# Kernel optimization log

Hardware: AMD Instinct MI355X
Metric: run time of the kernel (lower is better)

Reference implementation:

```python
import jax, jax.numpy as jnp
import numpy as np

N = 100000   # nodes per batched graph
E = 1000000  # edges per batched graph
G = 64       # graphs in batch
D = 64       # node feature dim
H = 128      # hidden dim
L = 3        # num GCN layers
EPS = 1e-5


def setup_inputs() -> dict:
    key = jax.random.key(0)
    ks = jax.random.split(key, 20)
    def xavier(k, shape):
        fan_in, fan_out = shape[0], shape[1]
        lim = np.sqrt(6.0 / (fan_in + fan_out)).astype(np.float32)
        return jax.random.uniform(k, shape, jnp.float32, -lim, lim)
    return {
        'kernel_x': jax.random.normal(ks[0], (N, D), jnp.float32),
        'kernel_edge_index': jax.random.randint(ks[1], (2, E), 0, N, jnp.int32),
        'kernel_batch': jnp.sort(jax.random.randint(ks[2], (N,), 0, G, jnp.int32)),
        'design_x': jax.random.normal(ks[3], (N, D), jnp.float32),
        'design_edge_index': jax.random.randint(ks[4], (2, E), 0, N, jnp.int32),
        'design_batch': jnp.sort(jax.random.randint(ks[5], (N,), 0, G, jnp.int32)),
        'pragma_count': 4,
        'enc_W': xavier(ks[6], (D, H)), 'enc_b': jnp.zeros((H,), jnp.float32),
        'conv_W': jnp.stack([xavier(ks[7 + i], (H, H)) for i in range(L)]),
        'conv_b': jnp.zeros((L, H), jnp.float32),
        'ln_w': jnp.ones((L, H), jnp.float32), 'ln_b': jnp.zeros((L, H), jnp.float32),
        'head_W1': xavier(ks[10], (2 * H, H)), 'head_b1': jnp.zeros((H,), jnp.float32),
        'head_W2': xavier(ks[11], (H, H // 2)), 'head_b2': jnp.zeros((H // 2,), jnp.float32),
        'head_W3': xavier(ks[12], (H // 2, 1)), 'head_b3': jnp.zeros((1,), jnp.float32),
    }


def _gcn(x, W, b, src, dst):
    # PyG GCNConv: x' = D^{-1/2} (A + I) D^{-1/2} (x W) + b
    n = x.shape[0]
    xw = x @ W
    loop = jnp.arange(n, dtype=src.dtype)
    s = jnp.concatenate([src, loop])
    d = jnp.concatenate([dst, loop])
    deg = jax.ops.segment_sum(jnp.ones_like(d, dtype=x.dtype), d, num_segments=n)
    dinv = jax.lax.rsqrt(deg)  # deg >= 1 due to self-loops
    norm = dinv[s] * dinv[d]                       # [E+N]
    msgs = xw[s] * norm[:, None]                   # gather-transform
    return jax.ops.segment_sum(msgs, d, num_segments=n) + b


def _graph_layernorm(x, w, b, batch, num_graphs):
    # PyG LayerNorm mode='graph': normalize over all nodes+channels per graph
    n, c = x.shape
    cnt = jax.ops.segment_sum(jnp.ones((n,), x.dtype), batch, num_segments=num_graphs) * c
    mean = jax.ops.segment_sum(x.sum(axis=1), batch, num_segments=num_graphs) / cnt
    xc = x - mean[batch][:, None]
    var = jax.ops.segment_sum((xc * xc).sum(axis=1), batch, num_segments=num_graphs) / cnt
    out = xc * jax.lax.rsqrt(var + EPS)[batch][:, None]
    return out * w + b


def _encode_graph(x, edge_index, batch, enc_W, enc_b, conv_W, conv_b, ln_w, ln_b):
    src, dst = edge_index[0], edge_index[1]
    h = x @ enc_W + enc_b
    for i in range(L):
        h = _gcn(h, conv_W[i], conv_b[i], src, dst)
        h = _graph_layernorm(h, ln_w[i], ln_b[i], batch, G)
        if i < L - 1:
            h = jax.nn.relu(h)
    return jax.ops.segment_sum(h, batch, num_segments=G)  # global_add_pool -> [G, H]


def reference(kernel_x, kernel_edge_index, kernel_batch,
              design_x, design_edge_index, design_batch, pragma_count,
              enc_W, enc_b, conv_W, conv_b, ln_w, ln_b,
              head_W1, head_b1, head_W2, head_b2, head_W3, head_b3):
    design_repr = _encode_graph(design_x, design_edge_index, design_batch,
                                enc_W, enc_b, conv_W, conv_b, ln_w, ln_b)
    kernel_repr = _encode_graph(kernel_x, kernel_edge_index, kernel_batch,
                                enc_W, enc_b, conv_W, conv_b, ln_w, ln_b)
    combined = jnp.concatenate([kernel_repr, design_repr], axis=-1)  # [G, 2H]
    h = jax.nn.relu(combined @ head_W1 + head_b1)  # dropout is identity at eval
    h = jax.nn.relu(h @ head_W2 + head_b2)
    return h @ head_W3 + head_b3  # delta_pred [G, 1]
```

## Files before the change

kernel.cpp:

```cpp
#include <hip/hip_runtime.h>


#define TPB 256
#define FILL_CHUNK 2048

typedef __attribute__((ext_vector_type(8))) short bf16x8;
typedef __attribute__((ext_vector_type(4))) float f32x4;

__device__ __forceinline__ float bf2f(unsigned short s) {
  unsigned int u = ((unsigned int)s) << 16;
  float f;
  __builtin_memcpy(&f, &u, 4);
  return f;
}

__device__ __forceinline__ unsigned short f2bf(float f) {
  unsigned int u;
  __builtin_memcpy(&u, &f, 4);
  u = (u + 0x7FFF + ((u >> 16) & 1)) >> 16;
  return (unsigned short)u;
}


__global__ __launch_bounds__(TPB) void count_dst_k(const int* __restrict__ dst,
                                                   int* __restrict__ cnt, int E) {
  int e = blockIdx.x * TPB + threadIdx.x;
  if (e < E) atomicAdd(&cnt[dst[e]], 1);
}

__global__ __launch_bounds__(TPB) void prep_node_k(const int* __restrict__ cnt,
                                                   float* __restrict__ dinv,
                                                   const int* __restrict__ batch,
                                                   int* __restrict__ gstart, int n, int G) {
  int i = blockIdx.x * TPB + threadIdx.x;
  if (i >= n) return;
  dinv[i] = 1.0f / sqrtf((float)cnt[i] + 1.0f);
  int b = batch[i];
  if (i == 0) {
    for (int g = 0; g <= b; ++g) gstart[g] = 0;
  } else {
    int pb = batch[i - 1];
    for (int g = pb + 1; g <= b; ++g) gstart[g] = i;
  }
  if (i == n - 1) {
    for (int g = b + 1; g <= G; ++g) gstart[g] = n;
  }
}


__global__ __launch_bounds__(TPB) void scan_partial_k(const int* __restrict__ cnt,
                                                      int* __restrict__ bsum, int n) {
  __shared__ int sd[TPB];
  int t = threadIdx.x, i0 = blockIdx.x * 512 + t * 2;
  int s = 0;
  if (i0 < n) s += cnt[i0];
  if (i0 + 1 < n) s += cnt[i0 + 1];
  sd[t] = s;
  __syncthreads();
  for (int st = TPB / 2; st > 0; st >>= 1) {
    if (t < st) sd[t] += sd[t + st];
    __syncthreads();
  }
  if (t == 0) bsum[blockIdx.x] = sd[0];
}

__global__ __launch_bounds__(TPB) void scan_small_k(const int* __restrict__ bsum,
                                                    int* __restrict__ bpre, int P,
                                                    int* __restrict__ rowptr, int n) {
  __shared__ int sd[TPB];
  int t = threadIdx.x;
  int v = (t < P) ? bsum[t] : 0;
  sd[t] = v;
  __syncthreads();
  for (int d = 1; d < TPB; d <<= 1) {
    int w = (t >= d) ? sd[t - d] : 0;
    __syncthreads();
    sd[t] += w;
    __syncthreads();
  }
  if (t < P) bpre[t] = sd[t] - v;
  if (t == TPB - 1) rowptr[n] = sd[TPB - 1];
}

__global__ __launch_bounds__(TPB) void scan_fill_k(const int* __restrict__ cnt,
                                                   const int* __restrict__ bpre,
                                                   int* __restrict__ rowptr,
                                                   int* __restrict__ cursor, int n) {
  __shared__ int sd[TPB];
  int t = threadIdx.x, i0 = blockIdx.x * 512 + t * 2;
  int c0 = (i0 < n) ? cnt[i0] : 0;
  int c1 = (i0 + 1 < n) ? cnt[i0 + 1] : 0;
  int s = c0 + c1;
  sd[t] = s;
  __syncthreads();
  for (int d = 1; d < TPB; d <<= 1) {
    int w = (t >= d) ? sd[t - d] : 0;
    __syncthreads();
    sd[t] += w;
    __syncthreads();
  }
  int ex = sd[t] - s + bpre[blockIdx.x];
  if (i0 < n) { rowptr[i0] = ex; cursor[i0] = ex; }
  if (i0 + 1 < n) { rowptr[i0 + 1] = ex + c0; cursor[i0 + 1] = ex + c0; }
}


__global__ __launch_bounds__(TPB) void csrfill_k(const int* __restrict__ esrc,
                                                 const int* __restrict__ edst,
                                                 int* __restrict__ cursor,
                                                 int* __restrict__ csr_src, int E, int n) {
  int range = blockIdx.x & 7;
  int chunk = blockIdx.x >> 3;
  int nper = (n + 7) >> 3;
  int lo = range * nper;
  int hi = lo + nper; if (hi > n) hi = n;
  int base = chunk * FILL_CHUNK;
  int end = base + FILL_CHUNK; if (end > E) end = E;
  for (int e = base + threadIdx.x; e < end; e += TPB) {
    int d = edst[e];
    if (d >= lo && d < hi) {
      int p = atomicAdd(&cursor[d], 1);
      csr_src[p] = esrc[e];
    }
  }
}


__global__ __launch_bounds__(TPB) void wprep_k(const float* __restrict__ encW,
                                               const float* __restrict__ convW,
                                               unsigned short* __restrict__ encWt,
                                               unsigned short* __restrict__ convWt) {
  int idx = blockIdx.x * TPB + threadIdx.x;
  if (idx < 64 * 128) {
    int k = idx >> 7, c = idx & 127;
    encWt[c * 64 + k] = f2bf(encW[idx]);
  }
  idx -= 64 * 128;
  if (idx >= 0 && idx < 3 * 128 * 128) {
    int l = idx >> 14, r = idx & 16383;
    int k = r >> 7, c = r & 127;
    convWt[l * 16384 + c * 128 + k] = f2bf(convW[idx]);
  }
}


template <int K, bool BIAS, bool LNRELU, bool SCALE, bool F32IN>
__global__ __launch_bounds__(TPB) void mfma_gemm_k(
    const void* __restrict__ Av, const unsigned short* __restrict__ Wt,
    const float* __restrict__ bias, unsigned short* __restrict__ C, int nrows,
    const int* __restrict__ batch, const float* __restrict__ meanA,
    const float* __restrict__ rsigA, const float* __restrict__ lnw,
    const float* __restrict__ lnb, const float* __restrict__ dinv) {
  __shared__ short As[128 * K];
  __shared__ short Bs[128 * K];
  const int tid = threadIdx.x;
  const int r0 = blockIdx.x << 7;
  const int lane = tid & 63;
  const int wv = tid >> 6;
  const int lr = lane & 15, lg = lane >> 4;
  constexpr int CPR = K / 8;

  for (int i = tid; i < 128 * CPR; i += TPB) {
    int rloc = i / CPR, cb = i % CPR;
    int r = r0 + rloc;
    bf16x8 v = {0, 0, 0, 0, 0, 0, 0, 0};
    if (r < nrows) {
      if (F32IN) {
        const float* Af = ((const float*)Av) + (long)r * K + cb * 8;
        float4 f0 = *(const float4*)Af;
        float4 f1 = *(const float4*)(Af + 4);
        v[0] = (short)f2bf(f0.x); v[1] = (short)f2bf(f0.y);
        v[2] = (short)f2bf(f0.z); v[3] = (short)f2bf(f0.w);
        v[4] = (short)f2bf(f1.x); v[5] = (short)f2bf(f1.y);
        v[6] = (short)f2bf(f1.z); v[7] = (short)f2bf(f1.w);
      } else {
        v = *(const bf16x8*)(((const unsigned short*)Av) + (long)r * K + cb * 8);
        if (LNRELU) {
          int g = batch[r];
          float m = meanA[g], rs = rsigA[g];
          int c0 = cb * 8;
#pragma unroll
          for (int j = 0; j < 8; ++j) {
            float f = bf2f((unsigned short)v[j]);
            f = (f - m) * rs * lnw[c0 + j] + lnb[c0 + j];
            f = fmaxf(f, 0.f);
            v[j] = (short)f2bf(f);
          }
        }
      }
    }
    int sb = cb ^ (rloc & 7);
    *(bf16x8*)(&As[rloc * K + sb * 8]) = v;
  }
  for (int i = tid; i < 128 * CPR; i += TPB) {
    int rloc = i / CPR, cb = i % CPR;
    bf16x8 v = *(const bf16x8*)(Wt + (long)rloc * K + cb * 8);
    int sb = cb ^ (rloc & 7);
    *(bf16x8*)(&Bs[rloc * K + sb * 8]) = v;
  }
  __syncthreads();

  f32x4 acc[2][8];
#pragma unroll
  for (int m = 0; m < 2; ++m)
#pragma unroll
    for (int n = 0; n < 8; ++n) acc[m][n] = {0.f, 0.f, 0.f, 0.f};

  const int wrow = wv * 32;
#pragma unroll
  for (int k0 = 0; k0 < K; k0 += 32) {
    const int cbk = (k0 >> 3) + lg;
    bf16x8 a[2], b[8];
#pragma unroll
    for (int m = 0; m < 2; ++m) {
      int rr = wrow + m * 16 + lr;
      int sb = cbk ^ (rr & 7);
      a[m] = *(const bf16x8*)(&As[rr * K + sb * 8]);
    }
#pragma unroll
    for (int n = 0; n < 8; ++n) {
      int rr = n * 16 + lr;
      int sb = cbk ^ (rr & 7);
      b[n] = *(const bf16x8*)(&Bs[rr * K + sb * 8]);
    }
#pragma unroll
    for (int m = 0; m < 2; ++m)
#pragma unroll
      for (int n = 0; n < 8; ++n)
        acc[m][n] = __builtin_amdgcn_mfma_f32_16x16x32_bf16(a[m], b[n], acc[m][n], 0, 0, 0);
  }

  float bv[8];
#pragma unroll
  for (int n = 0; n < 8; ++n) bv[n] = BIAS ? bias[n * 16 + lr] : 0.f;
#pragma unroll
  for (int m = 0; m < 2; ++m) {
#pragma unroll
    for (int ri = 0; ri < 4; ++ri) {
      int r = r0 + wrow + m * 16 + lg * 4 + ri;
      if (r < nrows) {
        float dv = SCALE ? dinv[r] : 1.f;
#pragma unroll
        for (int n = 0; n < 8; ++n) {
          float v = acc[m][n][ri] + bv[n];
          if (SCALE) v *= dv;
          C[(long)r * 128 + n * 16 + lr] = f2bf(v);
        }
      }
    }
  }
}


__global__ __launch_bounds__(TPB) void aggregate_k(
    const uint4* __restrict__ xws, const int* __restrict__ rowptr,
    const int* __restrict__ csr, const float* __restrict__ dinv,
    const float* __restrict__ bias, uint4* __restrict__ outb,
    float2* __restrict__ rs2, int n) {
  int wave = threadIdx.x >> 6, lane = threadIdx.x & 63;
  int d = (blockIdx.x << 2) + wave;
  if (d >= n) return;
  const int g3 = lane >> 4, cpos = lane & 15;
  float acc[8];
#pragma unroll
  for (int j = 0; j < 8; ++j) acc[j] = 0.f;

  int p0 = rowptr[d], p1 = rowptr[d + 1];
  for (int base = p0; base < p1; base += 64) {
    int idx = base + lane;
    int sl = (idx < p1) ? csr[idx] : 0;
    int cnt = p1 - base;
    if (cnt > 64) cnt = 64;
    for (int e = 0; e < cnt; e += 8) {
      int e0 = e + g3, e1 = e + 4 + g3;
      int s0 = __shfl(sl, e0);
      int s1 = __shfl(sl, e1);
      uint4 u0 = xws[(long)s0 * 16 + cpos];
      uint4 u1 = xws[(long)s1 * 16 + cpos];
      if (e0 < cnt) {
        acc[0] += __uint_as_float(u0.x << 16);
        acc[1] += __uint_as_float(u0.x & 0xffff0000u);
        acc[2] += __uint_as_float(u0.y << 16);
        acc[3] += __uint_as_float(u0.y & 0xffff0000u);
        acc[4] += __uint_as_float(u0.z << 16);
        acc[5] += __uint_as_float(u0.z & 0xffff0000u);
        acc[6] += __uint_as_float(u0.w << 16);
        acc[7] += __uint_as_float(u0.w & 0xffff0000u);
      }
      if (e1 < cnt) {
        acc[0] += __uint_as_float(u1.x << 16);
        acc[1] += __uint_as_float(u1.x & 0xffff0000u);
        acc[2] += __uint_as_float(u1.y << 16);
        acc[3] += __uint_as_float(u1.y & 0xffff0000u);
        acc[4] += __uint_as_float(u1.z << 16);
        acc[5] += __uint_as_float(u1.z & 0xffff0000u);
        acc[6] += __uint_as_float(u1.w << 16);
        acc[7] += __uint_as_float(u1.w & 0xffff0000u);
      }
    }
  }

#pragma unroll
  for (int j = 0; j < 8; ++j) {
    acc[j] += __shfl_xor(acc[j], 16);
    acc[j] += __shfl_xor(acc[j], 32);
  }

  uint4 su = xws[(long)d * 16 + cpos];
  float dd = dinv[d];
  float sv[8];
  sv[0] = __uint_as_float(su.x << 16);
  sv[1] = __uint_as_float(su.x & 0xffff0000u);
  sv[2] = __uint_as_float(su.y << 16);
  sv[3] = __uint_as_float(su.y & 0xffff0000u);
  sv[4] = __uint_as_float(su.z << 16);
  sv[5] = __uint_as_float(su.z & 0xffff0000u);
  sv[6] = __uint_as_float(su.w << 16);
  sv[7] = __uint_as_float(su.w & 0xffff0000u);
  const float4* b4 = (const float4*)bias;
  float4 bb0 = b4[cpos * 2];
  float4 bb1 = b4[cpos * 2 + 1];
  float val[8];
  val[0] = (acc[0] + sv[0]) * dd + bb0.x;
  val[1] = (acc[1] + sv[1]) * dd + bb0.y;
  val[2] = (acc[2] + sv[2]) * dd + bb0.z;
  val[3] = (acc[3] + sv[3]) * dd + bb0.w;
  val[4] = (acc[4] + sv[4]) * dd + bb1.x;
  val[5] = (acc[5] + sv[5]) * dd + bb1.y;
  val[6] = (acc[6] + sv[6]) * dd + bb1.z;
  val[7] = (acc[7] + sv[7]) * dd + bb1.w;

  if (g3 == 0) {
    uint4 o;
    o.x = (unsigned)f2bf(val[0]) | ((unsigned)f2bf(val[1]) << 16);
    o.y = (unsigned)f2bf(val[2]) | ((unsigned)f2bf(val[3]) << 16);
    o.z = (unsigned)f2bf(val[4]) | ((unsigned)f2bf(val[5]) << 16);
    o.w = (unsigned)f2bf(val[6]) | ((unsigned)f2bf(val[7]) << 16);
    outb[(long)d * 16 + cpos] = o;
  }

  float s1 = 0.f, s2 = 0.f;
#pragma unroll
  for (int j = 0; j < 8; ++j) {
    s1 += val[j];
    s2 += val[j] * val[j];
  }
#pragma unroll
  for (int m = 8; m >= 1; m >>= 1) {
    s1 += __shfl_xor(s1, m);
    s2 += __shfl_xor(s2, m);
  }
  if (lane == 0) rs2[d] = make_float2(s1, s2);
}


__global__ __launch_bounds__(TPB) void gstats_k(const float2* __restrict__ rs2,
                                                const int* __restrict__ gstart,
                                                float* __restrict__ meanA,
                                                float* __restrict__ rsigA,
                                                float* __restrict__ cntA) {
  __shared__ double sd1[TPB], sd2[TPB];
  int g = blockIdx.x, t = threadIdx.x;
  int n0 = gstart[g], n1 = gstart[g + 1];
  double s1 = 0, s2 = 0;
  for (int i = n0 + t; i < n1; i += TPB) {
    float2 v = rs2[i];
    s1 += v.x; s2 += v.y;
  }
  sd1[t] = s1; sd2[t] = s2;
  __syncthreads();
  for (int st = TPB / 2; st > 0; st >>= 1) {
    if (t < st) { sd1[t] += sd1[t + st]; sd2[t] += sd2[t + st]; }
    __syncthreads();
  }
  if (t == 0) {
    double cntd = (double)(n1 - n0) * 128.0;
    if (cntd > 0.0) {
      double mean = sd1[0] / cntd;
      double var = sd2[0] / cntd - mean * mean;
      if (var < 0.0) var = 0.0;
      meanA[g] = (float)mean;
      rsigA[g] = (float)(1.0 / sqrt(var + 1e-5));
    } else {
      meanA[g] = 0.f;
      rsigA[g] = 0.f;
    }
    cntA[g] = (float)(n1 - n0);
  }
}


typedef __attribute__((ext_vector_type(8))) unsigned short u16x8;

__global__ __launch_bounds__(TPB) void pool_k(const unsigned short* __restrict__ x,
                                              const int* __restrict__ gstart,
                                              float* __restrict__ part) {
  __shared__ float red[16][132];
  int g = blockIdx.x >> 3, s = blockIdx.x & 7;
  int tid = threadIdx.x;
  int ro = tid >> 4, c8 = tid & 15;
  int n0 = gstart[g], n1 = gstart[g + 1];
  float acc[8];
#pragma unroll
  for (int j = 0; j < 8; ++j) acc[j] = 0.f;
  for (int nn = n0 + s + ro * 8; nn < n1; nn += 8 * 16) {
    u16x8 v = *(const u16x8*)(x + (long)nn * 128 + c8 * 8);
#pragma unroll
    for (int j = 0; j < 8; ++j) acc[j] += bf2f(v[j]);
  }
#pragma unroll
  for (int j = 0; j < 8; ++j) red[ro][c8 * 8 + j] = acc[j];
  __syncthreads();
  for (int st = 8; st > 0; st >>= 1) {
    if (ro < st) {
#pragma unroll
      for (int j = 0; j < 8; ++j) red[ro][c8 * 8 + j] += red[ro + st][c8 * 8 + j];
    }
    __syncthreads();
  }
  if (tid < 128) part[((long)s * 64 + g) * 128 + tid] = red[0][tid];
}


__global__ __launch_bounds__(TPB) void head_k(
    const float* __restrict__ partK, const float* __restrict__ partD,
    const float* __restrict__ meanF, const float* __restrict__ rsigF,
    const float* __restrict__ cntF, const float* __restrict__ lnw2,
    const float* __restrict__ lnb2, const float* __restrict__ W1,
    const float* __restrict__ b1, const float* __restrict__ W2,
    const float* __restrict__ b2, const float* __restrict__ W3,
    const float* __restrict__ b3, float* __restrict__ out) {
  __shared__ float ps[256];
  __shared__ float part[256];
  __shared__ float h1[128];
  __shared__ float h2[64];
  int g = blockIdx.x, tid = threadIdx.x;
  {
    int j = tid & 127, side = tid >> 7;
    const float* pp = side ? partD : partK;
    float S = 0.f;
#pragma unroll
    for (int s = 0; s < 8; ++s) S += pp[((long)s * 64 + g) * 128 + j];
    float m = meanF[side * 64 + g], r = rsigF[side * 64 + g], c = cntF[side * 64 + g];
    ps[tid] = lnw2[j] * r * (S - m * c) + lnb2[j] * c;
  }
  __syncthreads();
  {
    int j = tid & 127, half = tid >> 7;
    float acc = 0.f;
    const float* w = W1 + (size_t)half * 128 * 128 + j;
    const float* p = ps + half * 128;
#pragma unroll 8
    for (int k = 0; k < 128; ++k) acc = fmaf(p[k], w[(size_t)k * 128], acc);
    part[tid] = acc;
    __syncthreads();
    if (tid < 128) h1[tid] = fmaxf(part[tid] + part[tid + 128] + b1[tid], 0.f);
    __syncthreads();
  }
  {
    int j = tid & 63, q = tid >> 6;
    float acc = 0.f;
    const float* w = W2 + (size_t)q * 32 * 64 + j;
    const float* p = h1 + q * 32;
#pragma unroll 8
    for (int k = 0; k < 32; ++k) acc = fmaf(p[k], w[(size_t)k * 64], acc);
    part[tid] = acc;
    __syncthreads();
    if (tid < 64)
      h2[tid] = fmaxf(part[tid] + part[tid + 64] + part[tid + 128] + part[tid + 192] + b2[tid], 0.f);
    __syncthreads();
  }
  if (tid < 64) {
    float v = h2[tid] * W3[tid];
#pragma unroll
    for (int m = 32; m >= 1; m >>= 1) v += __shfl_xor(v, m);
    if (tid == 0) out[g] = v + b3[0];
  }
}


extern "C" void kernel_launch(void* const* d_in, const int* in_sizes, int n_in,
                              void* d_out, int out_size, void* d_ws, size_t ws_size,
                              hipStream_t stream) {
  const int N = in_sizes[2];
  const int E = in_sizes[1] / 2;
  const int G = 64, H = 128, D = 64, L = 3;
  (void)n_in; (void)ws_size; (void)D; (void)out_size;

  const float* kernel_x = (const float*)d_in[0];
  const int* kernel_ei  = (const int*)d_in[1];
  const int* kernel_b   = (const int*)d_in[2];
  const float* design_x = (const float*)d_in[3];
  const int* design_ei  = (const int*)d_in[4];
  const int* design_b   = (const int*)d_in[5];
  const float* encW  = (const float*)d_in[7];
  const float* encB  = (const float*)d_in[8];
  const float* convW = (const float*)d_in[9];
  const float* convB = (const float*)d_in[10];
  const float* lnw   = (const float*)d_in[11];
  const float* lnb   = (const float*)d_in[12];
  const float* W1 = (const float*)d_in[13];
  const float* b1 = (const float*)d_in[14];
  const float* W2 = (const float*)d_in[15];
  const float* b2 = (const float*)d_in[16];
  const float* W3 = (const float*)d_in[17];
  const float* b3 = (const float*)d_in[18];
  float* out = (float*)d_out;

  char* ws = (char*)d_ws;
  size_t off = 0;
  auto alloc = [&](size_t bytes) -> void* {
    void* p = ws + off;
    off = (off + bytes + 511) & ~(size_t)511;
    return p;
  };
  unsigned short* hb   = (unsigned short*)alloc((size_t)N * H * 2);
  unsigned short* bufX = (unsigned short*)alloc((size_t)N * H * 2);
  unsigned short* bufY = (unsigned short*)alloc((size_t)N * H * 2);
  float* dinv    = (float*)alloc((size_t)N * 4);
  int* cntI      = (int*)alloc((size_t)N * 4);
  int* rowptr    = (int*)alloc((size_t)(N + 1) * 4);
  int* cursor    = (int*)alloc((size_t)N * 4);
  int* csr_src   = (int*)alloc((size_t)E * 4);
  int* gstart    = (int*)alloc((size_t)(G + 1) * 4);
  float2* rs2    = (float2*)alloc((size_t)N * 8);
  float* meanS   = (float*)alloc((size_t)G * 4);
  float* rsigS   = (float*)alloc((size_t)G * 4);
  float* cntS    = (float*)alloc((size_t)G * 4);
  float* meanF   = (float*)alloc((size_t)2 * G * 4);
  float* rsigF   = (float*)alloc((size_t)2 * G * 4);
  float* cntF    = (float*)alloc((size_t)2 * G * 4);
  float* partK   = (float*)alloc((size_t)8 * G * 128 * 4);
  float* partD   = (float*)alloc((size_t)8 * G * 128 * 4);
  int* bsum      = (int*)alloc(512 * 4);
  int* bpre      = (int*)alloc(512 * 4);
  unsigned short* encWt  = (unsigned short*)alloc((size_t)128 * 64 * 2);
  unsigned short* convWt = (unsigned short*)alloc((size_t)L * 128 * 128 * 2);

  const int gN    = (N + TPB - 1) / TPB;
  const int gE    = (E + TPB - 1) / TPB;
  const int gGemm = (N + 127) / 128;
  const int gAgg  = (N + 3) / 4;
  const int P     = (N + 511) / 512;
  const int gFill = 8 * ((E + FILL_CHUNK - 1) / FILL_CHUNK);

  wprep_k<<<(64 * 128 + 3 * 128 * 128 + TPB - 1) / TPB, TPB, 0, stream>>>(
      encW, convW, encWt, convWt);

  struct GraphIn { const float* x; const int* ei; const int* batch; };
  GraphIn graphs[2] = {
      {kernel_x, kernel_ei, kernel_b},
      {design_x, design_ei, design_b},
  };

  for (int gi = 0; gi < 2; ++gi) {
    const float* x = graphs[gi].x;
    const int* esrc = graphs[gi].ei;
    const int* edst = graphs[gi].ei + E;
    const int* batch = graphs[gi].batch;

    hipMemsetAsync(cntI, 0, (size_t)N * 4, stream);
    count_dst_k<<<gE, TPB, 0, stream>>>(edst, cntI, E);
    prep_node_k<<<gN, TPB, 0, stream>>>(cntI, dinv, batch, gstart, N, G);
    scan_partial_k<<<P, TPB, 0, stream>>>(cntI, bsum, N);
    scan_small_k<<<1, TPB, 0, stream>>>(bsum, bpre, P, rowptr, N);
    scan_fill_k<<<P, TPB, 0, stream>>>(cntI, bpre, rowptr, cursor, N);
    csrfill_k<<<gFill, TPB, 0, stream>>>(esrc, edst, cursor, csr_src, E, N);

    mfma_gemm_k<64, true, false, false, true><<<gGemm, TPB, 0, stream>>>(
        x, encWt, encB, hb, N, nullptr, nullptr, nullptr, nullptr, nullptr, nullptr);

    for (int i = 0; i < L; ++i) {
      const unsigned short* src = (i == 0) ? hb : bufY;
      float* mS = (i == L - 1) ? meanF + gi * G : meanS;
      float* rS = (i == L - 1) ? rsigF + gi * G : rsigS;
      float* cS = (i == L - 1) ? cntF + gi * G : cntS;
      if (i == 0)
        mfma_gemm_k<128, false, false, true, false><<<gGemm, TPB, 0, stream>>>(
            src, convWt + (size_t)i * H * H, nullptr, bufX, N,
            nullptr, nullptr, nullptr, nullptr, nullptr, dinv);
      else
        mfma_gemm_k<128, false, true, true, false><<<gGemm, TPB, 0, stream>>>(
            src, convWt + (size_t)i * H * H, nullptr, bufX, N,
            batch, meanS, rsigS, lnw + (size_t)(i - 1) * H,
            lnb + (size_t)(i - 1) * H, dinv);
      aggregate_k<<<gAgg, TPB, 0, stream>>>((const uint4*)bufX, rowptr, csr_src,
                                            dinv, convB + (size_t)i * H,
                                            (uint4*)bufY, rs2, N);
      gstats_k<<<G, TPB, 0, stream>>>(rs2, gstart, mS, rS, cS);
    }
    pool_k<<<G * 8, TPB, 0, stream>>>(bufY, gstart, gi ? partD : partK);
  }

  head_k<<<G, TPB, 0, stream>>>(partK, partD, meanF, rsigF, cntF,
                                lnw + (size_t)(L - 1) * H, lnb + (size_t)(L - 1) * H,
                                W1, b1, W2, b2, W3, b3, out);
}
```

Baseline: 703.4 us.

## Batch kernel and design graphs into one merged graph pass

Concatenates the two input graphs into a single 2N-node, 2E-edge graph with offset node indices and graph ids 64..127, so every preprocessing, GEMM, aggregation, stats and pooling kernel launches once instead of twice. This halves the number of kernel launches and doubles the work per launch, which should improve GPU occupancy on the smaller kernels. The cost is a few branches per element to pick which input is being read. The code hardcodes 100000 and 64 as offsets, and the single-block scan now needs 512 threads to cover the larger partial-sum count.

```diff
diff --git a/kernel.cpp b/kernel.cpp
--- a/kernel.cpp
+++ b/kernel.cpp
@@ -5,6 +5,7 @@
 #define FILL_CHUNK 2048
 
 typedef __attribute__((ext_vector_type(8))) short bf16x8;
+typedef __attribute__((ext_vector_type(8))) unsigned short u16x8;
 typedef __attribute__((ext_vector_type(4))) float f32x4;
 
 __device__ __forceinline__ float bf2f(unsigned short s) {
@@ -22,28 +23,35 @@
 }
 
 
-__global__ __launch_bounds__(TPB) void count_dst_k(const int* __restrict__ dst,
+__global__ __launch_bounds__(TPB) void count_dst_k(const int* __restrict__ kei,
+                                                   const int* __restrict__ dei,
                                                    int* __restrict__ cnt, int E) {
   int e = blockIdx.x * TPB + threadIdx.x;
-  if (e < E) atomicAdd(&cnt[dst[e]], 1);
+  if (e >= 2 * E) return;
+  int d = (e < E) ? kei[E + e] : dei[e] + 100000;
+  atomicAdd(&cnt[d], 1);
 }
 
 __global__ __launch_bounds__(TPB) void prep_node_k(const int* __restrict__ cnt,
                                                    float* __restrict__ dinv,
-                                                   const int* __restrict__ batch,
-                                                   int* __restrict__ gstart, int n, int G) {
+                                                   const int* __restrict__ kb,
+                                                   const int* __restrict__ db,
+                                                   int* __restrict__ batchU,
+                                                   int* __restrict__ gstart,
+                                                   int N, int NT) {
   int i = blockIdx.x * TPB + threadIdx.x;
-  if (i >= n) return;
+  if (i >= NT) return;
   dinv[i] = 1.0f / sqrtf((float)cnt[i] + 1.0f);
-  int b = batch[i];
+  int b = (i < N) ? kb[i] : db[i - N] + 64;
+  batchU[i] = b;
   if (i == 0) {
     for (int g = 0; g <= b; ++g) gstart[g] = 0;
   } else {
-    int pb = batch[i - 1];
+    int pb = (i - 1 < N) ? kb[i - 1] : db[i - 1 - N] + 64;
     for (int g = pb + 1; g <= b; ++g) gstart[g] = i;
   }
-  if (i == n - 1) {
-    for (int g = b + 1; g <= G; ++g) gstart[g] = n;
+  if (i == NT - 1) {
+    for (int g = b + 1; g <= 128; ++g) gstart[g] = NT;
   }
 }
 
@@ -64,22 +72,22 @@
   if (t == 0) bsum[blockIdx.x] = sd[0];
 }
 
-__global__ __launch_bounds__(TPB) void scan_small_k(const int* __restrict__ bsum,
+__global__ __launch_bounds__(512) void scan_small_k(const int* __restrict__ bsum,
                                                     int* __restrict__ bpre, int P,
                                                     int* __restrict__ rowptr, int n) {
-  __shared__ int sd[TPB];
+  __shared__ int sd[512];
   int t = threadIdx.x;
   int v = (t < P) ? bsum[t] : 0;
   sd[t] = v;
   __syncthreads();
-  for (int d = 1; d < TPB; d <<= 1) {
+  for (int d = 1; d < 512; d <<= 1) {
     int w = (t >= d) ? sd[t - d] : 0;
     __syncthreads();
     sd[t] += w;
     __syncthreads();
   }
   if (t < P) bpre[t] = sd[t] - v;
-  if (t == TPB - 1) rowptr[n] = sd[TPB - 1];
+  if (t == 511) rowptr[n] = sd[511];
 }
 
 __global__ __launch_bounds__(TPB) void scan_fill_k(const int* __restrict__ cnt,
@@ -105,22 +113,26 @@
 }
 
 
-__global__ __launch_bounds__(TPB) void csrfill_k(const int* __restrict__ esrc,
-                                                 const int* __restrict__ edst,
+__global__ __launch_bounds__(TPB) void csrfill_k(const int* __restrict__ kei,
+                                                 const int* __restrict__ dei,
                                                  int* __restrict__ cursor,
-                                                 int* __restrict__ csr_src, int E, int n) {
+                                                 int* __restrict__ csr_src,
+                                                 int E, int NT) {
   int range = blockIdx.x & 7;
   int chunk = blockIdx.x >> 3;
-  int nper = (n + 7) >> 3;
+  int nper = (NT + 7) >> 3;
   int lo = range * nper;
-  int hi = lo + nper; if (hi > n) hi = n;
+  int hi = lo + nper; if (hi > NT) hi = NT;
   int base = chunk * FILL_CHUNK;
-  int end = base + FILL_CHUNK; if (end > E) end = E;
+  int end = base + FILL_CHUNK; if (end > 2 * E) end = 2 * E;
+  const int N = NT >> 1;
   for (int e = base + threadIdx.x; e < end; e += TPB) {
-    int d = edst[e];
+    int s, d;
+    if (e < E) { s = kei[e]; d = kei[E + e]; }
+    else       { s = dei[e - E] + N; d = dei[e] + N; }
     if (d >= lo && d < hi) {
       int p = atomicAdd(&cursor[d], 1);
-      csr_src[p] = esrc[e];
+      csr_src[p] = s;
     }
   }
 }
@@ -146,7 +158,9 @@
 
 template <int K, bool BIAS, bool LNRELU, bool SCALE, bool F32IN>
 __global__ __launch_bounds__(TPB) void mfma_gemm_k(
-    const void* __restrict__ Av, const unsigned short* __restrict__ Wt,
+    const unsigned short* __restrict__ A, const float* __restrict__ X1,
+    const float* __restrict__ X2, int nsplit,
+    const unsigned short* __restrict__ Wt,
     const float* __restrict__ bias, unsigned short* __restrict__ C, int nrows,
     const int* __restrict__ batch, const float* __restrict__ meanA,
     const float* __restrict__ rsigA, const float* __restrict__ lnw,
@@ -166,7 +180,7 @@
     bf16x8 v = {0, 0, 0, 0, 0, 0, 0, 0};
     if (r < nrows) {
       if (F32IN) {
-        const float* Af = ((const float*)Av) + (long)r * K + cb * 8;
+        const float* Af = (r < nsplit ? X1 + (long)r * K : X2 + (long)(r - nsplit) * K) + cb * 8;
         float4 f0 = *(const float4*)Af;
         float4 f1 = *(const float4*)(Af + 4);
         v[0] = (short)f2bf(f0.x); v[1] = (short)f2bf(f0.y);
@@ -174,7 +188,7 @@
         v[4] = (short)f2bf(f1.x); v[5] = (short)f2bf(f1.y);
         v[6] = (short)f2bf(f1.z); v[7] = (short)f2bf(f1.w);
       } else {
-        v = *(const bf16x8*)(((const unsigned short*)Av) + (long)r * K + cb * 8);
+        v = *(const bf16x8*)(A + (long)r * K + cb * 8);
         if (LNRELU) {
           int g = batch[r];
           float m = meanA[g], rs = rsigA[g];
@@ -390,8 +404,6 @@
 }
 
 
-typedef __attribute__((ext_vector_type(8))) unsigned short u16x8;
-
 __global__ __launch_bounds__(TPB) void pool_k(const unsigned short* __restrict__ x,
                                               const int* __restrict__ gstart,
                                               float* __restrict__ part) {
@@ -418,30 +430,30 @@
     }
     __syncthreads();
   }
-  if (tid < 128) part[((long)s * 64 + g) * 128 + tid] = red[0][tid];
+  if (tid < 128) part[((long)s * 128 + g) * 128 + tid] = red[0][tid];
 }
 
 
 __global__ __launch_bounds__(TPB) void head_k(
-    const float* __restrict__ partK, const float* __restrict__ partD,
-    const float* __restrict__ meanF, const float* __restrict__ rsigF,
-    const float* __restrict__ cntF, const float* __restrict__ lnw2,
-    const float* __restrict__ lnb2, const float* __restrict__ W1,
-    const float* __restrict__ b1, const float* __restrict__ W2,
-    const float* __restrict__ b2, const float* __restrict__ W3,
-    const float* __restrict__ b3, float* __restrict__ out) {
+    const float* __restrict__ part, const float* __restrict__ meanU,
+    const float* __restrict__ rsigU, const float* __restrict__ cntU,
+    const float* __restrict__ lnw2, const float* __restrict__ lnb2,
+    const float* __restrict__ W1, const float* __restrict__ b1,
+    const float* __restrict__ W2, const float* __restrict__ b2,
+    const float* __restrict__ W3, const float* __restrict__ b3,
+    float* __restrict__ out) {
   __shared__ float ps[256];
-  __shared__ float part[256];
+  __shared__ float prt[256];
   __shared__ float h1[128];
   __shared__ float h2[64];
   int g = blockIdx.x, tid = threadIdx.x;
   {
     int j = tid & 127, side = tid >> 7;
-    const float* pp = side ? partD : partK;
+    int gg = side ? 64 + g : g;
     float S = 0.f;
 #pragma unroll
-    for (int s = 0; s < 8; ++s) S += pp[((long)s * 64 + g) * 128 + j];
-    float m = meanF[side * 64 + g], r = rsigF[side * 64 + g], c = cntF[side * 64 + g];
+    for (int s = 0; s < 8; ++s) S += part[((long)s * 128 + gg) * 128 + j];
+    float m = meanU[gg], r = rsigU[gg], c = cntU[gg];
     ps[tid] = lnw2[j] * r * (S - m * c) + lnb2[j] * c;
   }
   __syncthreads();
@@ -452,9 +464,9 @@
     const float* p = ps + half * 128;
 #pragma unroll 8
     for (int k = 0; k < 128; ++k) acc = fmaf(p[k], w[(size_t)k * 128], acc);
-    part[tid] = acc;
-    __syncthreads();
-    if (tid < 128) h1[tid] = fmaxf(part[tid] + part[tid + 128] + b1[tid], 0.f);
+    prt[tid] = acc;
+    __syncthreads();
+    if (tid < 128) h1[tid] = fmaxf(prt[tid] + prt[tid + 128] + b1[tid], 0.f);
     __syncthreads();
   }
   {
@@ -464,10 +476,10 @@
     const float* p = h1 + q * 32;
 #pragma unroll 8
     for (int k = 0; k < 32; ++k) acc = fmaf(p[k], w[(size_t)k * 64], acc);
-    part[tid] = acc;
+    prt[tid] = acc;
     __syncthreads();
     if (tid < 64)
-      h2[tid] = fmaxf(part[tid] + part[tid + 64] + part[tid + 128] + part[tid + 192] + b2[tid], 0.f);
+      h2[tid] = fmaxf(prt[tid] + prt[tid + 64] + prt[tid + 128] + prt[tid + 192] + b2[tid], 0.f);
     __syncthreads();
   }
   if (tid < 64) {
@@ -484,8 +496,9 @@
                               hipStream_t stream) {
   const int N = in_sizes[2];
   const int E = in_sizes[1] / 2;
-  const int G = 64, H = 128, D = 64, L = 3;
-  (void)n_in; (void)ws_size; (void)D; (void)out_size;
+  const int NT = 2 * N, ET = 2 * E;
+  const int H = 128, L = 3;
+  (void)n_in; (void)ws_size; (void)out_size;
 
   const float* kernel_x = (const float*)d_in[0];
   const int* kernel_ei  = (const int*)d_in[1];
@@ -514,85 +527,72 @@
     off = (off + bytes + 511) & ~(size_t)511;
     return p;
   };
-  unsigned short* hb   = (unsigned short*)alloc((size_t)N * H * 2);
-  unsigned short* bufX = (unsigned short*)alloc((size_t)N * H * 2);
-  unsigned short* bufY = (unsigned short*)alloc((size_t)N * H * 2);
-  float* dinv    = (float*)alloc((size_t)N * 4);
-  int* cntI      = (int*)alloc((size_t)N * 4);
-  int* rowptr    = (int*)alloc((size_t)(N + 1) * 4);
-  int* cursor    = (int*)alloc((size_t)N * 4);
-  int* csr_src   = (int*)alloc((size_t)E * 4);
-  int* gstart    = (int*)alloc((size_t)(G + 1) * 4);
-  float2* rs2    = (float2*)alloc((size_t)N * 8);
-  float* meanS   = (float*)alloc((size_t)G * 4);
-  float* rsigS   = (float*)alloc((size_t)G * 4);
-  float* cntS    = (float*)alloc((size_t)G * 4);
-  float* meanF   = (float*)alloc((size_t)2 * G * 4);
-  float* rsigF   = (float*)alloc((size_t)2 * G * 4);
-  float* cntF    = (float*)alloc((size_t)2 * G * 4);
-  float* partK   = (float*)alloc((size_t)8 * G * 128 * 4);
-  float* partD   = (float*)alloc((size_t)8 * G * 128 * 4);
+  unsigned short* bufA = (unsigned short*)alloc((size_t)NT * H * 2);
+  unsigned short* bufX = (unsigned short*)alloc((size_t)NT * H * 2);
+  float* dinv    = (float*)alloc((size_t)NT * 4);
+  int* cntI      = (int*)alloc((size_t)NT * 4);
+  int* rowptr    = (int*)alloc((size_t)(NT + 1) * 4);
+  int* cursor    = (int*)alloc((size_t)NT * 4);
+  int* csr_src   = (int*)alloc((size_t)ET * 4);
+  int* batchU    = (int*)alloc((size_t)NT * 4);
+  int* gstart    = (int*)alloc((size_t)129 * 4);
+  float2* rs2    = (float2*)alloc((size_t)NT * 8);
+  float* meanS   = (float*)alloc((size_t)128 * 4);
+  float* rsigS   = (float*)alloc((size_t)128 * 4);
+  float* cntS    = (float*)alloc((size_t)128 * 4);
+  float* meanU   = (float*)alloc((size_t)128 * 4);
+  float* rsigU   = (float*)alloc((size_t)128 * 4);
+  float* cntU    = (float*)alloc((size_t)128 * 4);
+  float* part    = (float*)alloc((size_t)8 * 128 * 128 * 4);
   int* bsum      = (int*)alloc(512 * 4);
   int* bpre      = (int*)alloc(512 * 4);
   unsigned short* encWt  = (unsigned short*)alloc((size_t)128 * 64 * 2);
   unsigned short* convWt = (unsigned short*)alloc((size_t)L * 128 * 128 * 2);
 
-  const int gN    = (N + TPB - 1) / TPB;
-  const int gE    = (E + TPB - 1) / TPB;
-  const int gGemm = (N + 127) / 128;
-  const int gAgg  = (N + 3) / 4;
-  const int P     = (N + 511) / 512;
-  const int gFill = 8 * ((E + FILL_CHUNK - 1) / FILL_CHUNK);
+  const int gNT   = (NT + TPB - 1) / TPB;
+  const int gET   = (ET + TPB - 1) / TPB;
+  const int gGemm = (NT + 127) / 128;
+  const int gAgg  = (NT + 3) / 4;
+  const int P     = (NT + 511) / 512;
+  const int gFill = 8 * ((ET + FILL_CHUNK - 1) / FILL_CHUNK);
 
   wprep_k<<<(64 * 128 + 3 * 128 * 128 + TPB - 1) / TPB, TPB, 0, stream>>>(
       encW, convW, encWt, convWt);
 
-  struct GraphIn { const float* x; const int* ei; const int* batch; };
-  GraphIn graphs[2] = {
-      {kernel_x, kernel_ei, kernel_b},
-      {design_x, design_ei, design_b},
-  };
-
-  for (int gi = 0; gi < 2; ++gi) {
-    const float* x = graphs[gi].x;
-    const int* esrc = graphs[gi].ei;
-    const int* edst = graphs[gi].ei + E;
-    const int* batch = graphs[gi].batch;
-
-    hipMemsetAsync(cntI, 0, (size_t)N * 4, stream);
-    count_dst_k<<<gE, TPB, 0, stream>>>(edst, cntI, E);
-    prep_node_k<<<gN, TPB, 0, stream>>>(cntI, dinv, batch, gstart, N, G);
-    scan_partial_k<<<P, TPB, 0, stream>>>(cntI, bsum, N);
-    scan_small_k<<<1, TPB, 0, stream>>>(bsum, bpre, P, rowptr, N);
-    scan_fill_k<<<P, TPB, 0, stream>>>(cntI, bpre, rowptr, cursor, N);
-    csrfill_k<<<gFill, TPB, 0, stream>>>(esrc, edst, cursor, csr_src, E, N);
-
-    mfma_gemm_k<64, true, false, false, true><<<gGemm, TPB, 0, stream>>>(
-        x, encWt, encB, hb, N, nullptr, nullptr, nullptr, nullptr, nullptr, nullptr);
-
-    for (int i = 0; i < L; ++i) {
-      const unsigned short* src = (i == 0) ? hb : bufY;
-      float* mS = (i == L - 1) ? meanF + gi * G : meanS;
-      float* rS = (i == L - 1) ? rsigF + gi * G : rsigS;
-      float* cS = (i == L - 1) ? cntF + gi * G : cntS;
-      if (i == 0)
-        mfma_gemm_k<128, false, false, true, false><<<gGemm, TPB, 0, stream>>>(
-            src, convWt + (size_t)i * H * H, nullptr, bufX, N,
-            nullptr, nullptr, nullptr, nullptr, nullptr, dinv);
-      else
-        mfma_gemm_k<128, false, true, true, false><<<gGemm, TPB, 0, stream>>>(
-            src, convWt + (size_t)i * H * H, nullptr, bufX, N,
-            batch, meanS, rsigS, lnw + (size_t)(i - 1) * H,
-            lnb + (size_t)(i - 1) * H, dinv);
-      aggregate_k<<<gAgg, TPB, 0, stream>>>((const uint4*)bufX, rowptr, csr_src,
-                                            dinv, convB + (size_t)i * H,
-                                            (uint4*)bufY, rs2, N);
-      gstats_k<<<G, TPB, 0, stream>>>(rs2, gstart, mS, rS, cS);
-    }
-    pool_k<<<G * 8, TPB, 0, stream>>>(bufY, gstart, gi ? partD : partK);
-  }
-
-  head_k<<<G, TPB, 0, stream>>>(partK, partD, meanF, rsigF, cntF,
-                                lnw + (size_t)(L - 1) * H, lnb + (size_t)(L - 1) * H,
-                                W1, b1, W2, b2, W3, b3, out);
-}
+  hipMemsetAsync(cntI, 0, (size_t)NT * 4, stream);
+  count_dst_k<<<gET, TPB, 0, stream>>>(kernel_ei, design_ei, cntI, E);
+  prep_node_k<<<gNT, TPB, 0, stream>>>(cntI, dinv, kernel_b, design_b, batchU,
+                                       gstart, N, NT);
+  scan_partial_k<<<P, TPB, 0, stream>>>(cntI, bsum, NT);
+  scan_small_k<<<1, 512, 0, stream>>>(bsum, bpre, P, rowptr, NT);
+  scan_fill_k<<<P, TPB, 0, stream>>>(cntI, bpre, rowptr, cursor, NT);
+  csrfill_k<<<gFill, TPB, 0, stream>>>(kernel_ei, design_ei, cursor, csr_src, E, NT);
+
+  mfma_gemm_k<64, true, false, false, true><<<gGemm, TPB, 0, stream>>>(
+      nullptr, kernel_x, design_x, N, encWt, encB, bufA, NT,
+      nullptr, nullptr, nullptr, nullptr, nullptr, nullptr);
+
+  for (int i = 0; i < L; ++i) {
+    float* mS = (i == L - 1) ? meanU : meanS;
+    float* rS = (i == L - 1) ? rsigU : rsigS;
+    float* cS = (i == L - 1) ? cntU : cntS;
+    if (i == 0)
+      mfma_gemm_k<128, false, false, true, false><<<gGemm, TPB, 0, stream>>>(
+          bufA, nullptr, nullptr, 0, convWt + (size_t)i * H * H, nullptr, bufX, NT,
+          nullptr, nullptr, nullptr, nullptr, nullptr, dinv);
+    else
+      mfma_gemm_k<128, false, true, true, false><<<gGemm, TPB, 0, stream>>>(
+          bufA, nullptr, nullptr, 0, convWt + (size_t)i * H * H, nullptr, bufX, NT,
+          batchU, meanS, rsigS, lnw + (size_t)(i - 1) * H,
+          lnb + (size_t)(i - 1) * H, dinv);
+    aggregate_k<<<gAgg, TPB, 0, stream>>>((const uint4*)bufX, rowptr, csr_src,
+                                          dinv, convB + (size_t)i * H,
+                                          (uint4*)bufA, rs2, NT);
+    gstats_k<<<128, TPB, 0, stream>>>(rs2, gstart, mS, rS, cS);
+  }
+  pool_k<<<128 * 8, TPB, 0, stream>>>(bufA, gstart, part);
+
+  head_k<<<64, TPB, 0, stream>>>(part, meanU, rsigU, cntU,
+                                 lnw + (size_t)(L - 1) * H, lnb + (size_t)(L - 1) * H,
+                                 W1, b1, W2, b2, W3, b3, out);
+}
```

Result: faster. 630.8 us (-10.3%).
